# Performance work log

Hardware: AMD Instinct MI355X
Metric: run time of the kernel (lower is better)

Reference implementation:

```python
import jax, jax.numpy as jnp
import numpy as np

L, D, H, B, T = 8, 1024, 16, 2, 1024
FF = 4 * D
STD = 0.02
EPS = 1e-5


def setup_inputs() -> dict:
    key = jax.random.key(0)
    ks = jax.random.split(key, 9)
    d = {}
    d['x'] = jax.random.normal(ks[0], (B, T, D), jnp.float32)
    d['Wq'] = jax.random.normal(ks[1], (L, D, D), jnp.float32) * STD
    d['Wk'] = jax.random.normal(ks[2], (L, D, D), jnp.float32) * STD
    d['Wv'] = jax.random.normal(ks[3], (L, D, D), jnp.float32) * STD
    d['Wo'] = jax.random.normal(ks[4], (L, D, D), jnp.float32) * STD
    d['bq'] = jnp.zeros((L, D), jnp.float32)
    d['bk'] = jnp.zeros((L, D), jnp.float32)
    d['bv'] = jnp.zeros((L, D), jnp.float32)
    d['bo'] = jnp.zeros((L, D), jnp.float32)
    d['ln1_g'] = jnp.ones((L, D), jnp.float32)
    d['ln1_b'] = jnp.zeros((L, D), jnp.float32)
    d['ln2_g'] = jnp.ones((L, D), jnp.float32)
    d['ln2_b'] = jnp.zeros((L, D), jnp.float32)
    d['W1'] = jax.random.normal(ks[5], (L, FF, D), jnp.float32) * STD
    d['b1'] = jnp.zeros((L, FF), jnp.float32)
    d['W2'] = jax.random.normal(ks[6], (L, D, FF), jnp.float32) * STD
    d['b2'] = jnp.zeros((L, D), jnp.float32)
    d['lnf_g'] = jnp.ones((D,), jnp.float32)
    d['lnf_b'] = jnp.zeros((D,), jnp.float32)
    d['Whead'] = jax.random.normal(ks[7], (D, D), jnp.float32) * STD
    return d


def layernorm(x, g, b):
    mu = jnp.mean(x, axis=-1, keepdims=True)
    var = jnp.mean(jnp.square(x - mu), axis=-1, keepdims=True)
    return (x - mu) * jax.lax.rsqrt(var + EPS) * g + b


def positional_encoding(t, d):
    pos = jnp.arange(t, dtype=jnp.float32)[:, None]            # [T,1]
    i = jnp.arange(d)[None, :]                                  # [1,D]
    rates = 1.0 / jnp.power(10000.0, (2 * (i // 2)).astype(jnp.float32) / d)
    a = pos * rates                                             # [T,D]
    return jnp.where(i % 2 == 0, jnp.sin(a), jnp.cos(a))        # sin even, cos odd


def reference(x, Wq, bq, Wk, bk, Wv, bv, Wo, bo, ln1_g, ln1_b, ln2_g, ln2_b,
              W1, b1, W2, b2, lnf_g, lnf_b, Whead):
    b_, t_, d_ = x.shape
    hd = d_ // H
    x = x + positional_encoding(t_, d_)[None]
    mask = jnp.tril(jnp.ones((t_, t_), bool))                   # causal
    scale = 1.0 / np.sqrt(hd)
    for l in range(L):
        h = layernorm(x, ln1_g[l], ln1_b[l])
        q = (jnp.einsum('btd,ed->bte', h, Wq[l]) + bq[l]).reshape(b_, t_, H, hd)
        k = (jnp.einsum('btd,ed->bte', h, Wk[l]) + bk[l]).reshape(b_, t_, H, hd)
        v = (jnp.einsum('btd,ed->bte', h, Wv[l]) + bv[l]).reshape(b_, t_, H, hd)
        att = jnp.einsum('bqhd,bkhd->bhqk', q, k) * scale       # [B,H,T,T]
        att = jnp.where(mask, att, -jnp.inf)
        p = jax.nn.softmax(att, axis=-1)
        y = jnp.einsum('bhqk,bkhd->bqhd', p, v).reshape(b_, t_, d_)
        y = jnp.einsum('btd,ed->bte', y, Wo[l]) + bo[l]
        x = x + y
        h = layernorm(x, ln2_g[l], ln2_b[l])
        m = jax.nn.gelu(jnp.einsum('btd,fd->btf', h, W1[l]) + b1[l], approximate=False)
        m = jnp.einsum('btf,df->btd', m, W2[l]) + b2[l]
        x = x + m
    x = layernorm(x, lnf_g, lnf_b)
    return jnp.einsum('btd,ed->bte', x, Whead)
```

## Files before the change

kernel.cpp:

```cpp
#include <hip/hip_runtime.h>
#include <hip/hip_bf16.h>
#include <math.h>

#define LAYERS 8
#define DMODEL 1024
#define NHEAD  16
#define HDIM   64
#define BATCH  2
#define SEQ    1024
#define FFDIM  4096
#define ROWS   (BATCH*SEQ)
#define DD     (DMODEL*DMODEL)

using s16x8 = __attribute__((ext_vector_type(8))) short;
using f32x4 = __attribute__((ext_vector_type(4))) float;

__device__ __forceinline__ short f2bf(float f) {
    union { float f; unsigned u; } v; v.f = f;
    unsigned r = v.u + 0x7fffu + ((v.u >> 16) & 1u);
    return (short)(r >> 16);
}

__global__ __launch_bounds__(256) void cvt_kernel(const float* __restrict__ in,
                                                  short* __restrict__ out, int n) {
    int i = (blockIdx.x * 256 + threadIdx.x) * 8;
    if (i >= n) return;
    float4 a = *(const float4*)(in + i);
    float4 b = *(const float4*)(in + i + 4);
    s16x8 o;
    o[0]=f2bf(a.x); o[1]=f2bf(a.y); o[2]=f2bf(a.z); o[3]=f2bf(a.w);
    o[4]=f2bf(b.x); o[5]=f2bf(b.y); o[6]=f2bf(b.z); o[7]=f2bf(b.w);
    *(s16x8*)(out + i) = o;
}

__global__ __launch_bounds__(256) void cvt_str_kernel(const float* __restrict__ in,
                                                      short* __restrict__ out,
                                                      int n, int lstride, int off) {
    int i = (blockIdx.x * 256 + threadIdx.x) * 8;
    if (i >= n) return;
    int l = i / DD, r = i - l * DD;
    float4 a = *(const float4*)(in + i);
    float4 b = *(const float4*)(in + i + 4);
    s16x8 o;
    o[0]=f2bf(a.x); o[1]=f2bf(a.y); o[2]=f2bf(a.z); o[3]=f2bf(a.w);
    o[4]=f2bf(b.x); o[5]=f2bf(b.y); o[6]=f2bf(b.z); o[7]=f2bf(b.w);
    *(s16x8*)(out + (size_t)l * lstride + off + r) = o;
}

__global__ __launch_bounds__(256) void bias_concat_kernel(const float* __restrict__ bq,
                                                          const float* __restrict__ bk,
                                                          const float* __restrict__ bv,
                                                          float* __restrict__ dst) {
    int idx = blockIdx.x * 256 + threadIdx.x;
    if (idx >= LAYERS * 3 * DMODEL) return;
    int l = idx / (3 * DMODEL), j = idx - l * 3 * DMODEL;
    float v;
    if (j < DMODEL)           v = bq[l * DMODEL + j];
    else if (j < 2 * DMODEL)  v = bk[l * DMODEL + j - DMODEL];
    else                      v = bv[l * DMODEL + j - 2 * DMODEL];
    dst[idx] = v;
}

__global__ __launch_bounds__(256) void posenc_kernel(const float* __restrict__ xin,
                                                     float* __restrict__ xout) {
    int idx = blockIdx.x * 256 + threadIdx.x;
    int d = idx & (DMODEL - 1);
    int t = (idx >> 10) & (SEQ - 1);
    float e = (float)(2 * (d >> 1)) * (1.0f / DMODEL);
    float rate = expf(-e * 9.210340371976184f);
    float a = (float)t * rate;
    float pe = (d & 1) ? cosf(a) : sinf(a);
    xout[idx] = xin[idx] + pe;
}

__global__ __launch_bounds__(256) void ln_kernel(const float* __restrict__ x,
                                                 const float* __restrict__ g,
                                                 const float* __restrict__ b,
                                                 short* __restrict__ out) {
    int row = blockIdx.x;
    const float* xr = x + (size_t)row * DMODEL;
    int tid = threadIdx.x;
    int d = tid * 4;
    float4 v = *(const float4*)&xr[d];
    float s  = v.x + v.y + v.z + v.w;
    float ss = v.x*v.x + v.y*v.y + v.z*v.z + v.w*v.w;
    #pragma unroll
    for (int off = 32; off >= 1; off >>= 1) {
        s  += __shfl_xor(s, off);
        ss += __shfl_xor(ss, off);
    }
    __shared__ float red[8];
    int wid = tid >> 6, lane = tid & 63;
    if (lane == 0) { red[wid] = s; red[4 + wid] = ss; }
    __syncthreads();
    s  = red[0] + red[1] + red[2] + red[3];
    ss = red[4] + red[5] + red[6] + red[7];
    float mu   = s * (1.0f / DMODEL);
    float var  = ss * (1.0f / DMODEL) - mu * mu;
    float rstd = rsqrtf(var + 1e-5f);
    short4 o;
    o.x = f2bf((v.x - mu) * rstd * g[d+0] + b[d+0]);
    o.y = f2bf((v.y - mu) * rstd * g[d+1] + b[d+1]);
    o.z = f2bf((v.z - mu) * rstd * g[d+2] + b[d+2]);
    o.w = f2bf((v.w - mu) * rstd * g[d+3] + b[d+3]);
    *(short4*)&out[(size_t)row * DMODEL + d] = o;
}

#define EPI_QKV   0
#define EPI_RESID 1
#define EPI_GELU  2
#define EPI_HEAD  3

template<int EPI, bool WBF, int KSPLIT>
__global__ __launch_bounds__(256)
void gemm_bt(const short* __restrict__ A, const void* __restrict__ Wp,
             const float* __restrict__ bias, void* __restrict__ outp,
             int N, int K, int col0) {
    __shared__ short lds_a[128 * 32];
    __shared__ short lds_w[64 * 32];
    int tid  = threadIdx.x;
    int lane = tid & 63, wid = tid >> 6;
    int wr = wid >> 1, wc = wid & 1;
    int ml = lane & 15, kg = (lane >> 4) * 8;
    int m0 = blockIdx.y * 128, n0 = blockIdx.x * 64;
    int Ks = K / KSPLIT, kb = blockIdx.z * Ks;

    f32x4 acc[4][2] = {};

    int srow = tid >> 2, sq = tid & 3;
    const short* Ab0 = A + (size_t)(m0 + srow) * K + kb + sq * 8;
    const short* Ab1 = Ab0 + (size_t)64 * K;
    short* la0 = &lds_a[tid * 8];
    short* la1 = &lds_a[tid * 8 + 2048];
    short* lw  = &lds_w[tid * 8];
    const short* Wb = WBF ? ((const short*)Wp + (size_t)(n0 + srow) * K + kb + sq * 8) : nullptr;
    const float* Wf = WBF ? nullptr : ((const float*)Wp + (size_t)(n0 + srow) * K + kb + sq * 8);

    int nk = Ks >> 5;
    for (int kt = 0; kt < nk; ++kt) {
        *(s16x8*)la0 = *(const s16x8*)(Ab0 + kt * 32);
        *(s16x8*)la1 = *(const s16x8*)(Ab1 + kt * 32);
        if constexpr (WBF) {
            *(s16x8*)lw = *(const s16x8*)(Wb + kt * 32);
        } else {
            float4 w0 = *(const float4*)(Wf + kt * 32);
            float4 w1 = *(const float4*)(Wf + kt * 32 + 4);
            s16x8 wv;
            wv[0]=f2bf(w0.x); wv[1]=f2bf(w0.y); wv[2]=f2bf(w0.z); wv[3]=f2bf(w0.w);
            wv[4]=f2bf(w1.x); wv[5]=f2bf(w1.y); wv[6]=f2bf(w1.z); wv[7]=f2bf(w1.w);
            *(s16x8*)lw = wv;
        }
        __syncthreads();

        s16x8 af[4], bf[2];
        #pragma unroll
        for (int i = 0; i < 4; i++)
            af[i] = *(const s16x8*)&lds_a[(wr * 64 + i * 16 + ml) * 32 + kg];
        #pragma unroll
        for (int j = 0; j < 2; j++)
            bf[j] = *(const s16x8*)&lds_w[(wc * 32 + j * 16 + ml) * 32 + kg];
        #pragma unroll
        for (int i = 0; i < 4; i++)
            #pragma unroll
            for (int j = 0; j < 2; j++)
                acc[i][j] = __builtin_amdgcn_mfma_f32_16x16x32_bf16(af[i], bf[j], acc[i][j], 0, 0, 0);
        __syncthreads();
    }

    #pragma unroll
    for (int i = 0; i < 4; i++) {
        #pragma unroll
        for (int j = 0; j < 2; j++) {
            #pragma unroll
            for (int r = 0; r < 4; r++) {
                int row = m0 + wr * 64 + i * 16 + (lane >> 4) * 4 + r;
                int col = n0 + wc * 32 + j * 16 + ml;
                float val = acc[i][j][r];
                if constexpr (EPI == EPI_QKV) {
                    val += bias[col];
                    int gcol = col + col0;
                    int sel = gcol >> 10, cc = gcol & (DMODEL - 1);
                    int hh = cc >> 6, dd = cc & (HDIM - 1);
                    int bb = row >> 10, t = row & (SEQ - 1);
                    ((short*)outp)[(size_t)sel * ROWS * DMODEL +
                                   (((size_t)bb * NHEAD + hh) * SEQ + t) * HDIM + dd] = f2bf(val);
                } else if constexpr (EPI == EPI_RESID) {
                    size_t o = (size_t)row * N + col;
                    if constexpr (KSPLIT == 1) {
                        ((float*)outp)[o] += val + bias[col];
                    } else {
                        float add = val + (blockIdx.z == 0 ? bias[col] : 0.0f);
                        atomicAdd(&((float*)outp)[o], add);
                    }
                } else if constexpr (EPI == EPI_GELU) {
                    val += bias[col];
                    float ge = 0.5f * val * (1.0f + erff(val * 0.70710678118654752f));
                    ((short*)outp)[(size_t)row * N + col] = f2bf(ge);
                } else {
                    ((float*)outp)[(size_t)row * N + col] = val;
                }
            }
        }
    }
}

__global__ __launch_bounds__(256)
void attn_kernel(const short* __restrict__ q, const short* __restrict__ kp,
                 const short* __restrict__ v, short* __restrict__ y) {
    __shared__ short lds_k[64 * 64];
    __shared__ short lds_vt[64 * 64];
    __shared__ short lds_p[4][16 * 64];
    int tid  = threadIdx.x;
    int lane = tid & 63, wid = tid >> 6;
    int ml = lane & 15, kg = (lane >> 4) * 8;
    int qt = blockIdx.x, bh = blockIdx.y;
    size_t base = (size_t)bh * SEQ * HDIM;

    int qrow = qt * 64 + wid * 16 + ml;
    s16x8 qf[2];
    #pragma unroll
    for (int kk = 0; kk < 2; kk++)
        qf[kk] = *(const s16x8*)&q[base + (size_t)qrow * HDIM + kk * 32 + kg];

    f32x4 yacc[4] = {};
    float mrow[4] = {-1e30f, -1e30f, -1e30f, -1e30f};
    float lrow[4] = {};

    int tr = tid >> 2, c0 = (tid & 3) * 16;
    for (int kt = 0; kt <= qt; ++kt) {
        const short* kbp = &kp[base + (size_t)(kt * 64 + tr) * HDIM];
        *(s16x8*)&lds_k[tr * 64 + c0]     = *(const s16x8*)&kbp[c0];
        *(s16x8*)&lds_k[tr * 64 + c0 + 8] = *(const s16x8*)&kbp[c0 + 8];
        const short* vbp = &v[base + (size_t)(kt * 64 + tr) * HDIM];
        s16x8 v0 = *(const s16x8*)&vbp[c0];
        s16x8 v1 = *(const s16x8*)&vbp[c0 + 8];
        #pragma unroll
        for (int j = 0; j < 8; j++) {
            lds_vt[(c0 + j) * 64 + tr]     = v0[j];
            lds_vt[(c0 + 8 + j) * 64 + tr] = v1[j];
        }
        __syncthreads();

        f32x4 s[4] = {};
        #pragma unroll
        for (int ni = 0; ni < 4; ni++)
            #pragma unroll
            for (int kk = 0; kk < 2; kk++) {
                s16x8 bfr = *(const s16x8*)&lds_k[(ni * 16 + ml) * 64 + kk * 32 + kg];
                s[ni] = __builtin_amdgcn_mfma_f32_16x16x32_bf16(qf[kk], bfr, s[ni], 0, 0, 0);
            }
        int qg = qt * 64 + wid * 16 + (lane >> 4) * 4;
        #pragma unroll
        for (int ni = 0; ni < 4; ni++)
            #pragma unroll
            for (int r = 0; r < 4; r++) {
                float fv = s[ni][r] * 0.125f;
                if (kt == qt) {
                    int tg = kt * 64 + ni * 16 + ml;
                    if (tg > qg + r) fv = -1e30f;
                }
                s[ni][r] = fv;
            }
        #pragma unroll
        for (int r = 0; r < 4; r++) {
            float m = fmaxf(fmaxf(s[0][r], s[1][r]), fmaxf(s[2][r], s[3][r]));
            #pragma unroll
            for (int off = 1; off < 16; off <<= 1) m = fmaxf(m, __shfl_xor(m, off));
            float mnew = fmaxf(mrow[r], m);
            float corr = __expf(mrow[r] - mnew);
            mrow[r] = mnew;
            float sum = 0.f;
            #pragma unroll
            for (int ni = 0; ni < 4; ni++) {
                float p = __expf(s[ni][r] - mnew);
                s[ni][r] = p;
                sum += p;
            }
            #pragma unroll
            for (int off = 1; off < 16; off <<= 1) sum += __shfl_xor(sum, off);
            lrow[r] = lrow[r] * corr + sum;
            #pragma unroll
            for (int ni = 0; ni < 4; ni++) yacc[ni][r] *= corr;
        }
        int prow = (lane >> 4) * 4;
        #pragma unroll
        for (int ni = 0; ni < 4; ni++)
            #pragma unroll
            for (int r = 0; r < 4; r++)
                lds_p[wid][(prow + r) * 64 + ni * 16 + ml] = f2bf(s[ni][r]);
        s16x8 pa[2];
        #pragma unroll
        for (int kk = 0; kk < 2; kk++)
            pa[kk] = *(const s16x8*)&lds_p[wid][ml * 64 + kk * 32 + kg];
        #pragma unroll
        for (int ni = 0; ni < 4; ni++)
            #pragma unroll
            for (int kk = 0; kk < 2; kk++) {
                s16x8 vb = *(const s16x8*)&lds_vt[(ni * 16 + ml) * 64 + kk * 32 + kg];
                yacc[ni] = __builtin_amdgcn_mfma_f32_16x16x32_bf16(pa[kk], vb, yacc[ni], 0, 0, 0);
            }
        __syncthreads();
    }

    int b = bh >> 4, h = bh & 15;
    #pragma unroll
    for (int ni = 0; ni < 4; ni++)
        #pragma unroll
        for (int r = 0; r < 4; r++) {
            int t = qt * 64 + wid * 16 + (lane >> 4) * 4 + r;
            float val = yacc[ni][r] / lrow[r];
            y[((size_t)b * SEQ + t) * DMODEL + h * HDIM + ni * 16 + ml] = f2bf(val);
        }
}

extern "C" void kernel_launch(void* const* d_in, const int* in_sizes, int n_in,
                              void* d_out, int out_size, void* d_ws, size_t ws_size,
                              hipStream_t stream) {
    const float* x_in  = (const float*)d_in[0];
    const float* Wq    = (const float*)d_in[1];
    const float* Wk    = (const float*)d_in[2];
    const float* Wv    = (const float*)d_in[3];
    const float* Wo    = (const float*)d_in[4];
    const float* bq    = (const float*)d_in[5];
    const float* bk    = (const float*)d_in[6];
    const float* bv    = (const float*)d_in[7];
    const float* bo    = (const float*)d_in[8];
    const float* ln1_g = (const float*)d_in[9];
    const float* ln1_b = (const float*)d_in[10];
    const float* ln2_g = (const float*)d_in[11];
    const float* ln2_b = (const float*)d_in[12];
    const float* W1    = (const float*)d_in[13];
    const float* b1    = (const float*)d_in[14];
    const float* W2    = (const float*)d_in[15];
    const float* b2    = (const float*)d_in[16];
    const float* lnf_g = (const float*)d_in[17];
    const float* lnf_b = (const float*)d_in[18];
    const float* Whead = (const float*)d_in[19];

    char* wp = (char*)d_ws;
    float* x  = (float*)wp; wp += (size_t)ROWS * DMODEL * 4;
    short* h  = (short*)wp; wp += (size_t)ROWS * DMODEL * 2;
    char* pool = wp;        wp += (size_t)ROWS * FFDIM * 2;
    short* qb = (short*)pool;
    short* kb = (short*)(pool + (size_t)ROWS * DMODEL * 2);
    short* vb = (short*)(pool + (size_t)ROWS * DMODEL * 4);
    short* yb = (short*)(pool + (size_t)ROWS * DMODEL * 6);
    short* mb = (short*)pool;

    const size_t NDD = (size_t)LAYERS * DD;
    const size_t NFD = (size_t)LAYERS * FFDIM * DMODEL;
    const size_t NHD = (size_t)DD;
    size_t act_bytes = (size_t)(wp - (char*)d_ws);
    size_t wb_bytes  = (3 * NDD + NDD + 2 * NFD + NHD) * 2 + (size_t)LAYERS * 3 * DMODEL * 4;
    bool use_bf = ws_size >= act_bytes + wb_bytes;

    short *wqkvb=0,*wob=0,*w1b=0,*w2b=0,*whb=0; float* bqkv=0;
    if (use_bf) {
        wqkvb = (short*)wp; wp += 3 * NDD * 2;
        wob   = (short*)wp; wp += NDD * 2;
        w1b   = (short*)wp; wp += NFD * 2;
        w2b   = (short*)wp; wp += NFD * 2;
        whb   = (short*)wp; wp += NHD * 2;
        bqkv  = (float*)wp; wp += (size_t)LAYERS * 3 * DMODEL * 4;
        cvt_str_kernel<<<(int)(NDD / 2048), 256, 0, stream>>>(Wq, wqkvb, (int)NDD, 3 * DD, 0);
        cvt_str_kernel<<<(int)(NDD / 2048), 256, 0, stream>>>(Wk, wqkvb, (int)NDD, 3 * DD, DD);
        cvt_str_kernel<<<(int)(NDD / 2048), 256, 0, stream>>>(Wv, wqkvb, (int)NDD, 3 * DD, 2 * DD);
        cvt_kernel<<<(int)(NDD / 2048), 256, 0, stream>>>(Wo, wob, (int)NDD);
        cvt_kernel<<<(int)(NFD / 2048), 256, 0, stream>>>(W1, w1b, (int)NFD);
        cvt_kernel<<<(int)(NFD / 2048), 256, 0, stream>>>(W2, w2b, (int)NFD);
        cvt_kernel<<<(int)(NHD / 2048), 256, 0, stream>>>(Whead, whb, (int)NHD);
        bias_concat_kernel<<<(LAYERS * 3 * DMODEL + 255) / 256, 256, 0, stream>>>(bq, bk, bv, bqkv);
    }

    posenc_kernel<<<ROWS * DMODEL / 256, 256, 0, stream>>>(x_in, x);

    for (int l = 0; l < LAYERS; ++l) {
        size_t wdd = (size_t)l * DD;
        size_t wfd = (size_t)l * FFDIM * DMODEL;
        ln_kernel<<<ROWS, 256, 0, stream>>>(x, ln1_g + l * DMODEL, ln1_b + l * DMODEL, h);
        if (use_bf) {
            gemm_bt<EPI_QKV,true,1><<<dim3(48, 16), 256, 0, stream>>>(
                h, wqkvb + (size_t)l * 3 * DD, bqkv + l * 3 * DMODEL, qb, 3 * DMODEL, DMODEL, 0);
        } else {
            gemm_bt<EPI_QKV,false,1><<<dim3(16, 16), 256, 0, stream>>>(h, Wq + wdd, bq + l * DMODEL, qb, DMODEL, DMODEL, 0);
            gemm_bt<EPI_QKV,false,1><<<dim3(16, 16), 256, 0, stream>>>(h, Wk + wdd, bk + l * DMODEL, qb, DMODEL, DMODEL, 1024);
            gemm_bt<EPI_QKV,false,1><<<dim3(16, 16), 256, 0, stream>>>(h, Wv + wdd, bv + l * DMODEL, qb, DMODEL, DMODEL, 2048);
        }
        attn_kernel<<<dim3(16, 32), 256, 0, stream>>>(qb, kb, vb, yb);
        if (use_bf) {
            gemm_bt<EPI_RESID,true,2><<<dim3(16, 16, 2), 256, 0, stream>>>(yb, wob + wdd, bo + l * DMODEL, x, DMODEL, DMODEL, 0);
        } else {
            gemm_bt<EPI_RESID,false,2><<<dim3(16, 16, 2), 256, 0, stream>>>(yb, Wo + wdd, bo + l * DMODEL, x, DMODEL, DMODEL, 0);
        }
        ln_kernel<<<ROWS, 256, 0, stream>>>(x, ln2_g + l * DMODEL, ln2_b + l * DMODEL, h);
        if (use_bf) {
            gemm_bt<EPI_GELU,true,1><<<dim3(64, 16), 256, 0, stream>>>(h, w1b + wfd, b1 + l * FFDIM, mb, FFDIM, DMODEL, 0);
            gemm_bt<EPI_RESID,true,2><<<dim3(16, 16, 2), 256, 0, stream>>>(mb, w2b + wfd, b2 + l * DMODEL, x, DMODEL, FFDIM, 0);
        } else {
            gemm_bt<EPI_GELU,false,1><<<dim3(64, 16), 256, 0, stream>>>(h, W1 + wfd, b1 + l * FFDIM, mb, FFDIM, DMODEL, 0);
            gemm_bt<EPI_RESID,false,2><<<dim3(16, 16, 2), 256, 0, stream>>>(mb, W2 + wfd, b2 + l * DMODEL, x, DMODEL, FFDIM, 0);
        }
    }
    ln_kernel<<<ROWS, 256, 0, stream>>>(x, lnf_g, lnf_b, h);
    if (use_bf) {
        gemm_bt<EPI_HEAD,true,1><<<dim3(16, 16), 256, 0, stream>>>(h, whb, nullptr, d_out, DMODEL, DMODEL, 0);
    } else {
        gemm_bt<EPI_HEAD,false,1><<<dim3(16, 16), 256, 0, stream>>>(h, Whead, nullptr, d_out, DMODEL, DMODEL, 0);
    }
}
```

Before: 2.074 ms.

## Use direct global-to-LDS loads and wider N tiles for QKV and FFN1 GEMMs

Replaces the register round-trip for bf16 tile staging with global_load_lds builtins that write straight into shared memory, and adds a TN template parameter so the QKV and W1 GEMMs use 128-wide N tiles (more MFMAs per A-tile load). This aims to cut VGPR traffic and load instructions and to improve A-operand reuse. The costs are fewer blocks for those GEMMs, more accumulator registers, and reliance on the per-wave LDS layout of the direct-load path matching the fragment reads.

```diff
diff --git a/kernel.cpp b/kernel.cpp
--- a/kernel.cpp
+++ b/kernel.cpp
@@ -19,6 +19,12 @@
     union { float f; unsigned u; } v; v.f = f;
     unsigned r = v.u + 0x7fffu + ((v.u >> 16) & 1u);
     return (short)(r >> 16);
+}
+
+__device__ __forceinline__ void gl_lds16(const short* g, short* lbase) {
+    __builtin_amdgcn_global_load_lds((const __attribute__((address_space(1))) void*)g,
+                                     (__attribute__((address_space(3))) void*)lbase,
+                                     16, 0, 0);
 }
 
 __global__ __launch_bounds__(256) void cvt_kernel(const float* __restrict__ in,
@@ -111,58 +117,72 @@
 #define EPI_GELU  2
 #define EPI_HEAD  3
 
-template<int EPI, bool WBF, int KSPLIT>
+template<int EPI, bool WBF, int KSPLIT, int TN>
 __global__ __launch_bounds__(256)
 void gemm_bt(const short* __restrict__ A, const void* __restrict__ Wp,
              const float* __restrict__ bias, void* __restrict__ outp,
              int N, int K, int col0) {
+    constexpr int NW = TN / 32;
     __shared__ short lds_a[128 * 32];
-    __shared__ short lds_w[64 * 32];
+    __shared__ short lds_w[TN * 32];
     int tid  = threadIdx.x;
     int lane = tid & 63, wid = tid >> 6;
     int wr = wid >> 1, wc = wid & 1;
     int ml = lane & 15, kg = (lane >> 4) * 8;
-    int m0 = blockIdx.y * 128, n0 = blockIdx.x * 64;
+    int m0 = blockIdx.y * 128, n0 = blockIdx.x * TN;
     int Ks = K / KSPLIT, kb = blockIdx.z * Ks;
 
-    f32x4 acc[4][2] = {};
+    f32x4 acc[4][NW] = {};
 
     int srow = tid >> 2, sq = tid & 3;
-    const short* Ab0 = A + (size_t)(m0 + srow) * K + kb + sq * 8;
-    const short* Ab1 = Ab0 + (size_t)64 * K;
-    short* la0 = &lds_a[tid * 8];
-    short* la1 = &lds_a[tid * 8 + 2048];
-    short* lw  = &lds_w[tid * 8];
-    const short* Wb = WBF ? ((const short*)Wp + (size_t)(n0 + srow) * K + kb + sq * 8) : nullptr;
-    const float* Wf = WBF ? nullptr : ((const float*)Wp + (size_t)(n0 + srow) * K + kb + sq * 8);
+    const short* Ag0 = A + (size_t)(m0 + srow) * K + kb + sq * 8;
+    const short* Ag1 = Ag0 + (size_t)64 * K;
+    short* la0 = &lds_a[wid * 512];
+    short* la1 = &lds_a[2048 + wid * 512];
+    short* lw0 = &lds_w[wid * 512];
+    const short* Wb0 = WBF ? ((const short*)Wp + (size_t)(n0 + srow) * K + kb + sq * 8) : nullptr;
+    const float* Wf0 = WBF ? nullptr : ((const float*)Wp + (size_t)(n0 + srow) * K + kb + sq * 8);
 
     int nk = Ks >> 5;
     for (int kt = 0; kt < nk; ++kt) {
-        *(s16x8*)la0 = *(const s16x8*)(Ab0 + kt * 32);
-        *(s16x8*)la1 = *(const s16x8*)(Ab1 + kt * 32);
         if constexpr (WBF) {
-            *(s16x8*)lw = *(const s16x8*)(Wb + kt * 32);
+            gl_lds16(Ag0 + kt * 32, la0);
+            gl_lds16(Ag1 + kt * 32, la1);
+            gl_lds16(Wb0 + kt * 32, lw0);
+            if constexpr (TN == 128)
+                gl_lds16(Wb0 + (size_t)64 * K + kt * 32, &lds_w[2048 + wid * 512]);
         } else {
-            float4 w0 = *(const float4*)(Wf + kt * 32);
-            float4 w1 = *(const float4*)(Wf + kt * 32 + 4);
+            *(s16x8*)&lds_a[tid * 8]        = *(const s16x8*)(Ag0 + kt * 32);
+            *(s16x8*)&lds_a[2048 + tid * 8] = *(const s16x8*)(Ag1 + kt * 32);
+            float4 w0 = *(const float4*)(Wf0 + kt * 32);
+            float4 w1 = *(const float4*)(Wf0 + kt * 32 + 4);
             s16x8 wv;
             wv[0]=f2bf(w0.x); wv[1]=f2bf(w0.y); wv[2]=f2bf(w0.z); wv[3]=f2bf(w0.w);
             wv[4]=f2bf(w1.x); wv[5]=f2bf(w1.y); wv[6]=f2bf(w1.z); wv[7]=f2bf(w1.w);
-            *(s16x8*)lw = wv;
+            *(s16x8*)&lds_w[tid * 8] = wv;
+            if constexpr (TN == 128) {
+                const float* Wf1 = Wf0 + (size_t)64 * K;
+                float4 u0 = *(const float4*)(Wf1 + kt * 32);
+                float4 u1 = *(const float4*)(Wf1 + kt * 32 + 4);
+                s16x8 uv;
+                uv[0]=f2bf(u0.x); uv[1]=f2bf(u0.y); uv[2]=f2bf(u0.z); uv[3]=f2bf(u0.w);
+                uv[4]=f2bf(u1.x); uv[5]=f2bf(u1.y); uv[6]=f2bf(u1.z); uv[7]=f2bf(u1.w);
+                *(s16x8*)&lds_w[2048 + tid * 8] = uv;
+            }
         }
         __syncthreads();
 
-        s16x8 af[4], bf[2];
+        s16x8 af[4], bf[NW];
         #pragma unroll
         for (int i = 0; i < 4; i++)
             af[i] = *(const s16x8*)&lds_a[(wr * 64 + i * 16 + ml) * 32 + kg];
         #pragma unroll
-        for (int j = 0; j < 2; j++)
-            bf[j] = *(const s16x8*)&lds_w[(wc * 32 + j * 16 + ml) * 32 + kg];
+        for (int j = 0; j < NW; j++)
+            bf[j] = *(const s16x8*)&lds_w[(wc * (TN / 2) + j * 16 + ml) * 32 + kg];
         #pragma unroll
         for (int i = 0; i < 4; i++)
             #pragma unroll
-            for (int j = 0; j < 2; j++)
+            for (int j = 0; j < NW; j++)
                 acc[i][j] = __builtin_amdgcn_mfma_f32_16x16x32_bf16(af[i], bf[j], acc[i][j], 0, 0, 0);
         __syncthreads();
     }
@@ -170,11 +190,11 @@
     #pragma unroll
     for (int i = 0; i < 4; i++) {
         #pragma unroll
-        for (int j = 0; j < 2; j++) {
+        for (int j = 0; j < NW; j++) {
             #pragma unroll
             for (int r = 0; r < 4; r++) {
                 int row = m0 + wr * 64 + i * 16 + (lane >> 4) * 4 + r;
-                int col = n0 + wc * 32 + j * 16 + ml;
+                int col = n0 + wc * (TN / 2) + j * 16 + ml;
                 float val = acc[i][j][r];
                 if constexpr (EPI == EPI_QKV) {
                     val += bias[col];
@@ -379,32 +399,32 @@
         size_t wfd = (size_t)l * FFDIM * DMODEL;
         ln_kernel<<<ROWS, 256, 0, stream>>>(x, ln1_g + l * DMODEL, ln1_b + l * DMODEL, h);
         if (use_bf) {
-            gemm_bt<EPI_QKV,true,1><<<dim3(48, 16), 256, 0, stream>>>(
+            gemm_bt<EPI_QKV,true,1,128><<<dim3(24, 16), 256, 0, stream>>>(
                 h, wqkvb + (size_t)l * 3 * DD, bqkv + l * 3 * DMODEL, qb, 3 * DMODEL, DMODEL, 0);
         } else {
-            gemm_bt<EPI_QKV,false,1><<<dim3(16, 16), 256, 0, stream>>>(h, Wq + wdd, bq + l * DMODEL, qb, DMODEL, DMODEL, 0);
-            gemm_bt<EPI_QKV,false,1><<<dim3(16, 16), 256, 0, stream>>>(h, Wk + wdd, bk + l * DMODEL, qb, DMODEL, DMODEL, 1024);
-            gemm_bt<EPI_QKV,false,1><<<dim3(16, 16), 256, 0, stream>>>(h, Wv + wdd, bv + l * DMODEL, qb, DMODEL, DMODEL, 2048);
+            gemm_bt<EPI_QKV,false,1,64><<<dim3(16, 16), 256, 0, stream>>>(h, Wq + wdd, bq + l * DMODEL, qb, DMODEL, DMODEL, 0);
+            gemm_bt<EPI_QKV,false,1,64><<<dim3(16, 16), 256, 0, stream>>>(h, Wk + wdd, bk + l * DMODEL, qb, DMODEL, DMODEL, 1024);
+            gemm_bt<EPI_QKV,false,1,64><<<dim3(16, 16), 256, 0, stream>>>(h, Wv + wdd, bv + l * DMODEL, qb, DMODEL, DMODEL, 2048);
         }
         attn_kernel<<<dim3(16, 32), 256, 0, stream>>>(qb, kb, vb, yb);
         if (use_bf) {
-            gemm_bt<EPI_RESID,true,2><<<dim3(16, 16, 2), 256, 0, stream>>>(yb, wob + wdd, bo + l * DMODEL, x, DMODEL, DMODEL, 0);
+            gemm_bt<EPI_RESID,true,2,64><<<dim3(16, 16, 2), 256, 0, stream>>>(yb, wob + wdd, bo + l * DMODEL, x, DMODEL, DMODEL, 0);
         } else {
-            gemm_bt<EPI_RESID,false,2><<<dim3(16, 16, 2), 256, 0, stream>>>(yb, Wo + wdd, bo + l * DMODEL, x, DMODEL, DMODEL, 0);
+            gemm_bt<EPI_RESID,false,2,64><<<dim3(16, 16, 2), 256, 0, stream>>>(yb, Wo + wdd, bo + l * DMODEL, x, DMODEL, DMODEL, 0);
         }
         ln_kernel<<<ROWS, 256, 0, stream>>>(x, ln2_g + l * DMODEL, ln2_b + l * DMODEL, h);
         if (use_bf) {
-            gemm_bt<EPI_GELU,true,1><<<dim3(64, 16), 256, 0, stream>>>(h, w1b + wfd, b1 + l * FFDIM, mb, FFDIM, DMODEL, 0);
-            gemm_bt<EPI_RESID,true,2><<<dim3(16, 16, 2), 256, 0, stream>>>(mb, w2b + wfd, b2 + l * DMODEL, x, DMODEL, FFDIM, 0);
+            gemm_bt<EPI_GELU,true,1,128><<<dim3(32, 16), 256, 0, stream>>>(h, w1b + wfd, b1 + l * FFDIM, mb, FFDIM, DMODEL, 0);
+            gemm_bt<EPI_RESID,true,2,64><<<dim3(16, 16, 2), 256, 0, stream>>>(mb, w2b + wfd, b2 + l * DMODEL, x, DMODEL, FFDIM, 0);
         } else {
-            gemm_bt<EPI_GELU,false,1><<<dim3(64, 16), 256, 0, stream>>>(h, W1 + wfd, b1 + l * FFDIM, mb, FFDIM, DMODEL, 0);
-            gemm_bt<EPI_RESID,false,2><<<dim3(16, 16, 2), 256, 0, stream>>>(mb, W2 + wfd, b2 + l * DMODEL, x, DMODEL, FFDIM, 0);
+            gemm_bt<EPI_GELU,false,1,128><<<dim3(32, 16), 256, 0, stream>>>(h, W1 + wfd, b1 + l * FFDIM, mb, FFDIM, DMODEL, 0);
+            gemm_bt<EPI_RESID,false,2,64><<<dim3(16, 16, 2), 256, 0, stream>>>(mb, W2 + wfd, b2 + l * DMODEL, x, DMODEL, FFDIM, 0);
         }
     }
     ln_kernel<<<ROWS, 256, 0, stream>>>(x, lnf_g, lnf_b, h);
     if (use_bf) {
-        gemm_bt<EPI_HEAD,true,1><<<dim3(16, 16), 256, 0, stream>>>(h, whb, nullptr, d_out, DMODEL, DMODEL, 0);
+        gemm_bt<EPI_HEAD,true,1,64><<<dim3(16, 16), 256, 0, stream>>>(h, whb, nullptr, d_out, DMODEL, DMODEL, 0);
     } else {
-        gemm_bt<EPI_HEAD,false,1><<<dim3(16, 16), 256, 0, stream>>>(h, Whead, nullptr, d_out, DMODEL, DMODEL, 0);
-    }
-}
+        gemm_bt<EPI_HEAD,false,1,64><<<dim3(16, 16), 256, 0, stream>>>(h, Whead, nullptr, d_out, DMODEL, DMODEL, 0);
+    }
+}
```

New measurement: 2.103 ms. About the same (+1.4%).
